# Kernel optimization log

Hardware: AMD Instinct MI355X
Metric: run time of the kernel (lower is better)

Reference implementation:

```python
import jax, jax.numpy as jnp
import numpy as np

DEG = np.float32(np.pi / 180.0)


def _m33(rows):
    # rows: 3 lists of 3 per-batch scalars [B] -> [B,3,3]
    return jnp.stack([jnp.stack(r, axis=-1) for r in rows], axis=-2)


def setup_inputs() -> dict:
    key = jax.random.key(0)
    k1, k2, k3, k4 = jax.random.split(key, 4)
    images = jax.random.uniform(k1, (32, 512, 512, 3), dtype=jnp.float32)
    geom_u = jax.random.uniform(k2, (32, 8), dtype=jnp.float32)
    color_u = jax.random.uniform(k3, (32, 4), dtype=jnp.float32)
    cutout_u = jax.random.uniform(k4, (32, 5), dtype=jnp.float32)
    return {"images": images, "geom_u": geom_u, "color_u": color_u, "cutout_u": cutout_u}


def reference(images, geom_u, color_u, cutout_u):
    B, H, W, C = images.shape
    f32 = jnp.float32

    # --- per-image geometric params (defaults of augment()) ---
    flip = geom_u[:, 0] > 0.5
    tilt = (geom_u[:, 1] * 2 - 1) * (15 * DEG)     # perspective around X
    pan = (geom_u[:, 2] * 2 - 1) * (15 * DEG)      # perspective around Y
    rot = (geom_u[:, 3] * 2 - 1) * (15 * DEG)      # in-plane rotation
    sc = 1.0 + (geom_u[:, 4] * 2 - 1) * 0.1        # isotropic scale
    tx = (geom_u[:, 5] * 2 - 1) * 0.2              # translation (0.1 of image = 0.2 in [-1,1])
    ty = (geom_u[:, 6] * 2 - 1) * 0.2

    z = jnp.zeros_like(rot)
    o = jnp.ones_like(rot)
    fx = jnp.where(flip, f32(-1.0), f32(1.0))
    F = _m33([[fx, z, z], [z, o, z], [z, z, o]])
    ct, st = jnp.cos(tilt), jnp.sin(tilt)
    Rx = _m33([[o, z, z], [z, ct, -st], [z, st, ct]])
    cp, sp = jnp.cos(pan), jnp.sin(pan)
    Ry = _m33([[cp, z, sp], [z, o, z], [-sp, z, cp]])
    cr, sr = jnp.cos(rot), jnp.sin(rot)
    RS = _m33([[sc * cr, -sc * sr, z], [sc * sr, sc * cr, z], [z, z, o]])
    T = _m33([[o, z, tx], [z, o, ty], [z, z, o]])
    # output -> input homography in normalized [-1,1] coords: translation after
    # rotation/scale after perspective after flip (application order of augment())
    M = T @ RS @ Rx @ Ry @ F  # [B,3,3]

    # --- single bilinear resample through the composed homography ---
    ys, xs = jnp.meshgrid(jnp.linspace(-1.0, 1.0, H, dtype=f32),
                          jnp.linspace(-1.0, 1.0, W, dtype=f32), indexing="ij")
    pts = jnp.stack([xs.ravel(), ys.ravel(), jnp.ones(H * W, dtype=f32)], axis=0)  # [3,N]
    src = jnp.einsum("bij,jn->bin", M, pts)  # [B,3,N]
    u = src[:, 0] / src[:, 2]
    v = src[:, 1] / src[:, 2]
    px = (u + 1.0) * 0.5 * (W - 1)
    py = (v + 1.0) * 0.5 * (H - 1)
    valid = (px >= 0) & (px <= W - 1) & (py >= 0) & (py <= H - 1)
    x0 = jnp.clip(jnp.floor(px), 0, W - 1)
    y0 = jnp.clip(jnp.floor(py), 0, H - 1)
    wx = (px - x0)[..., None]
    wy = (py - y0)[..., None]
    x0i = x0.astype(jnp.int32)
    y0i = y0.astype(jnp.int32)
    x1i = jnp.clip(x0i + 1, 0, W - 1)
    y1i = jnp.clip(y0i + 1, 0, H - 1)
    b = jnp.arange(B)[:, None]
    g00 = images[b, y0i, x0i]  # [B,N,3]
    g01 = images[b, y0i, x1i]
    g10 = images[b, y1i, x0i]
    g11 = images[b, y1i, x1i]
    samp = (g00 * (1 - wx) * (1 - wy) + g01 * wx * (1 - wy)
            + g10 * (1 - wx) * wy + g11 * wx * wy)
    samp = samp * valid[..., None].astype(f32)  # zero fill outside
    x = samp.reshape(B, H, W, C)

    # --- color chain: gamma, then fused hue/saturation/brightness matrix ---
    gamma = 1.0 + (color_u[:, 3] * 2 - 1) * 0.2
    x = jnp.power(jnp.clip(x, 0.0, 1.0), gamma[:, None, None, None])

    theta = (color_u[:, 0] * 2 - 1) * (10 * DEG)
    c, s = jnp.cos(theta), jnp.sin(theta)
    a = f32(1.0 / np.sqrt(3.0))
    I3 = jnp.eye(3, dtype=f32)
    K = jnp.array([[0, -a, a], [a, 0, -a], [-a, a, 0]], dtype=f32)  # cross-product w/ gray axis
    A = jnp.full((3, 3), 1.0 / 3.0, dtype=f32)
    Rh = c[:, None, None] * I3 + s[:, None, None] * K + (1 - c)[:, None, None] * A  # hue rotation
    sat = 1.0 + (color_u[:, 1] * 2 - 1) * 0.4
    lum = jnp.array([0.299, 0.587, 0.114], dtype=f32)
    L = jnp.broadcast_to(lum, (3, 3))
    Sm = sat[:, None, None] * I3 + (1 - sat)[:, None, None] * L  # saturation
    bright = 1.0 + (color_u[:, 2] * 2 - 1) * 0.1
    Mc = bright[:, None, None] * (Sm @ Rh)  # [B,3,3]
    x = jnp.clip(jnp.einsum("bhwc,bdc->bhwd", x, Mc), 0.0, 1.0)

    # --- cutout (p=0.5, side in [0.3,0.5] of image) ---
    apply = cutout_u[:, 0] < 0.5
    cx, cy = cutout_u[:, 1], cutout_u[:, 2]
    cw = 0.3 + 0.2 * cutout_u[:, 3]
    ch = 0.3 + 0.2 * cutout_u[:, 4]
    gy, gx = jnp.meshgrid(jnp.linspace(0.0, 1.0, H, dtype=f32),
                          jnp.linspace(0.0, 1.0, W, dtype=f32), indexing="ij")
    mask = (apply[:, None, None]
            & (jnp.abs(gx[None] - cx[:, None, None]) < cw[:, None, None] * 0.5)
            & (jnp.abs(gy[None] - cy[:, None, None]) < ch[:, None, None] * 0.5))
    x = jnp.where(mask[..., None], f32(0.0), x)
    return x
```

## Files before the change

### kernel.cpp

```cpp
#include <hip/hip_runtime.h>
#include <math.h>

#define NB 32
#define HDIM 512
#define WDIM 512
#define HW (HDIM * WDIM)
#define PSTR 32
#define LIN11_OFF 1024
#define LIN01_OFF 1536

struct __attribute__((packed, aligned(4))) F3 { float x, y, z; };

__device__ inline void mm3(float* C, const float* A, const float* B) {
#pragma unroll
  for (int i = 0; i < 3; ++i) {
#pragma unroll
    for (int j = 0; j < 3; ++j) {
      float acc = __fmaf_rn(A[i*3+0], B[0*3+j], 0.0f);
      acc = __fmaf_rn(A[i*3+1], B[1*3+j], acc);
      acc = __fmaf_rn(A[i*3+2], B[2*3+j], acc);
      C[i*3+j] = acc;
    }
  }
}

__global__ void setup_params(const float* __restrict__ geom,
                             const float* __restrict__ color,
                             const float* __restrict__ cut,
                             float* __restrict__ W) {
  const int t = threadIdx.x;
  W[LIN11_OFF + t] = (float)((double)t * (2.0 / 511.0) + (-1.0));
  W[LIN01_OFF + t] = (float)((double)t * (1.0 / 511.0));
  if (t >= NB) return;
  const int b = t;

  const float DEGf = (float)(3.14159265358979323846 / 180.0);
  const float a15  = 15.0f * DEGf;
  const float a10  = 10.0f * DEGf;

  const float* g = geom + b * 8;
  float tilt = __fmul_rn(__fsub_rn(__fmul_rn(g[1], 2.0f), 1.0f), a15);
  float pan  = __fmul_rn(__fsub_rn(__fmul_rn(g[2], 2.0f), 1.0f), a15);
  float rotf = __fmul_rn(__fsub_rn(__fmul_rn(g[3], 2.0f), 1.0f), a15);
  float sc   = __fadd_rn(1.0f,
                 __fmul_rn(__fsub_rn(__fmul_rn(g[4], 2.0f), 1.0f), 0.1f));
  float tx   = __fmul_rn(__fsub_rn(__fmul_rn(g[5], 2.0f), 1.0f), 0.2f);
  float ty   = __fmul_rn(__fsub_rn(__fmul_rn(g[6], 2.0f), 1.0f), 0.2f);
  float fx   = (g[0] > 0.5f) ? -1.0f : 1.0f;

  float ct = (float)cos((double)tilt), st = (float)sin((double)tilt);
  float cp = (float)cos((double)pan),  sp = (float)sin((double)pan);
  float cr = (float)cos((double)rotf), sr = (float)sin((double)rotf);

  float sccr = __fmul_rn(sc, cr);
  float scsr = __fmul_rn(sc, sr);

  float F[9]  = {fx, 0.f, 0.f,  0.f, 1.f, 0.f,  0.f, 0.f, 1.f};
  float Rx[9] = {1.f, 0.f, 0.f,  0.f, ct, -st,  0.f, st, ct};
  float Ry[9] = {cp, 0.f, sp,  0.f, 1.f, 0.f,  -sp, 0.f, cp};
  float RS[9] = {sccr, -scsr, 0.f,  scsr, sccr, 0.f,  0.f, 0.f, 1.f};
  float T[9]  = {1.f, 0.f, tx,  0.f, 1.f, ty,  0.f, 0.f, 1.f};

  float t1[9], t2[9], M[9];
  mm3(t1, T, RS);
  mm3(t2, t1, Rx);
  mm3(t1, t2, Ry);
  mm3(M, t1, F);

  const float* c = color + b * 4;
  float theta  = __fmul_rn(__fsub_rn(__fmul_rn(c[0], 2.0f), 1.0f), a10);
  float sat    = __fadd_rn(1.0f,
                   __fmul_rn(__fsub_rn(__fmul_rn(c[1], 2.0f), 1.0f), 0.4f));
  float bright = __fadd_rn(1.0f,
                   __fmul_rn(__fsub_rn(__fmul_rn(c[2], 2.0f), 1.0f), 0.1f));
  float gammaf = __fadd_rn(1.0f,
                   __fmul_rn(__fsub_rn(__fmul_rn(c[3], 2.0f), 1.0f), 0.2f));

  float cth = (float)cos((double)theta), sth = (float)sin((double)theta);
  float omc = __fsub_rn(1.0f, cth);
  float oms = __fsub_rn(1.0f, sat);
  const float aK = (float)(1.0 / sqrt(3.0));
  const float Af = (float)(1.0 / 3.0);
  const float K[9]   = {0.f, -aK, aK,  aK, 0.f, -aK,  -aK, aK, 0.f};
  const float lum[3] = {(float)0.299, (float)0.587, (float)0.114};

  float Rh[9], Sm[9], SR[9];
#pragma unroll
  for (int i = 0; i < 3; ++i) {
#pragma unroll
    for (int j = 0; j < 3; ++j) {
      float I = (i == j) ? 1.0f : 0.0f;
      Rh[i*3+j] = __fadd_rn(
          __fadd_rn(__fmul_rn(cth, I), __fmul_rn(sth, K[i*3+j])),
          __fmul_rn(omc, Af));
      Sm[i*3+j] = __fadd_rn(__fmul_rn(sat, I), __fmul_rn(oms, lum[j]));
    }
  }
  mm3(SR, Sm, Rh);

  float* pp = W + b * PSTR;
#pragma unroll
  for (int i = 0; i < 9; ++i) pp[i] = M[i];
#pragma unroll
  for (int i = 0; i < 9; ++i) pp[9 + i] = __fmul_rn(bright, SR[i]);
  pp[18] = gammaf;

  const float* cu = cut + b * 5;
  pp[19] = (cu[0] < 0.5f) ? 1.0f : 0.0f;
  pp[20] = cu[1];
  pp[21] = cu[2];
  pp[22] = __fmul_rn(__fadd_rn(0.3f, __fmul_rn(0.2f, cu[3])), 0.5f);
  pp[23] = __fmul_rn(__fadd_rn(0.3f, __fmul_rn(0.2f, cu[4])), 0.5f);
}

__global__ __launch_bounds__(512, 1) void augment_kernel(
    const float* __restrict__ img, const float* __restrict__ W,
    float* __restrict__ out) {
  const int bkid = ((blockIdx.x & 7) << 9) | ((int)blockIdx.x >> 3);
  const int bb = bkid >> 7;
  const int tile = bkid & 127;
  const int t = (int)threadIdx.x;
  const int xx  = ((tile & 15) << 5) | (t & 31);
  const int yy0 = ((tile >> 4) << 6) | ((t >> 5) << 2);

  const float* pp = W + bb * PSTR;
  const float m00 = pp[0], m01 = pp[1], m02 = pp[2];
  const float m10 = pp[3], m11 = pp[4], m12 = pp[5];
  const float m20 = pp[6], m21 = pp[7], m22 = pp[8];

  const float xs = W[LIN11_OFF + xx];
  const float4 ysv = *(const float4*)(W + LIN11_OFF + yy0);
  const float ysa[4] = {ysv.x, ysv.y, ysv.z, ysv.w};

  const float m00xs = __fmul_rn(m00, xs);
  const float m10xs = __fmul_rn(m10, xs);
  const float m20xs = __fmul_rn(m20, xs);

  float wxa[4], wya[4], vma[4];
  int o00[4], o01[4], o10[4], o11[4];
#pragma unroll
  for (int i = 0; i < 4; ++i) {
    const float ys = ysa[i];
    const float s0 = __fadd_rn(
        __fadd_rn(m00xs, __fmul_rn(m01, ys)), m02);
    const float s1 = __fadd_rn(
        __fadd_rn(m10xs, __fmul_rn(m11, ys)), m12);
    const float s2 = __fadd_rn(
        __fadd_rn(m20xs, __fmul_rn(m21, ys)), m22);
    const float u = __fdiv_rn(s0, s2);
    const float v = __fdiv_rn(s1, s2);
    const float px = __fmul_rn(__fmul_rn(__fadd_rn(u, 1.0f), 0.5f), 511.0f);
    const float py = __fmul_rn(__fmul_rn(__fadd_rn(v, 1.0f), 0.5f), 511.0f);

    vma[i] =
        (px >= 0.0f && px <= 511.0f && py >= 0.0f && py <= 511.0f) ? 1.0f
                                                                   : 0.0f;
    const float pxc = __builtin_amdgcn_fmed3f(px, 0.0f, 511.0f);
    const float pyc = __builtin_amdgcn_fmed3f(py, 0.0f, 511.0f);
    const float x0f = floorf(pxc), y0f = floorf(pyc);
    wxa[i] = pxc - x0f;
    wya[i] = pyc - y0f;
    const int x0 = (int)x0f, y0 = (int)y0f;
    const int x1 = min(x0 + 1, WDIM - 1);
    const int y1 = min(y0 + 1, HDIM - 1);
    o00[i] = (y0 * WDIM + x0) * 3;
    o01[i] = (y0 * WDIM + x1) * 3;
    o10[i] = (y1 * WDIM + x0) * 3;
    o11[i] = (y1 * WDIM + x1) * 3;
  }

  const float* base = img + (size_t)bb * (HW * 3);
  F3 g00[4], g01[4], g10[4], g11[4];
#pragma unroll
  for (int i = 0; i < 4; ++i) {
    g00[i] = *(const F3*)(base + o00[i]);
    g01[i] = *(const F3*)(base + o01[i]);
    g10[i] = *(const F3*)(base + o10[i]);
    g11[i] = *(const F3*)(base + o11[i]);
  }
  __builtin_amdgcn_sched_barrier(0);

  const float c00 = pp[9],  c01 = pp[10], c02 = pp[11];
  const float c10 = pp[12], c11 = pp[13], c12 = pp[14];
  const float c20 = pp[15], c21 = pp[16], c22 = pp[17];
  const float gamma = pp[18];
  const float capply = pp[19], ccx = pp[20], ccy = pp[21];
  const float chw = pp[22], chh = pp[23];

  const float gx = W[LIN01_OFF + xx];
  const float4 gyv = *(const float4*)(W + LIN01_OFF + yy0);
  const float gya[4] = {gyv.x, gyv.y, gyv.z, gyv.w};
  const bool cutx = (capply != 0.0f) && (fabsf(__fsub_rn(gx, ccx)) < chw);

  const size_t pix0 = (size_t)bb * HW + (size_t)yy0 * WDIM + xx;
#pragma unroll
  for (int i = 0; i < 4; ++i) {
    const float wx = wxa[i], wy = wya[i], vm = vma[i];
    const float ax = (1.0f - wx) * vm;
    const float bx = wx * vm;
    const float w00 = ax * (1.0f - wy);
    const float w01 = bx * (1.0f - wy);
    const float w10 = ax * wy;
    const float w11 = bx * wy;

    float s, r0, r1, r2;
    s = g00[i].x * w00 + g01[i].x * w01 + g10[i].x * w10 + g11[i].x * w11;
    s = __builtin_amdgcn_fmed3f(s, 0.0f, 1.0f);
    r0 = __builtin_amdgcn_exp2f(gamma * __builtin_amdgcn_logf(s));
    s = g00[i].y * w00 + g01[i].y * w01 + g10[i].y * w10 + g11[i].y * w11;
    s = __builtin_amdgcn_fmed3f(s, 0.0f, 1.0f);
    r1 = __builtin_amdgcn_exp2f(gamma * __builtin_amdgcn_logf(s));
    s = g00[i].z * w00 + g01[i].z * w01 + g10[i].z * w10 + g11[i].z * w11;
    s = __builtin_amdgcn_fmed3f(s, 0.0f, 1.0f);
    r2 = __builtin_amdgcn_exp2f(gamma * __builtin_amdgcn_logf(s));

    float q0 = __builtin_amdgcn_fmed3f(c00 * r0 + c01 * r1 + c02 * r2, 0.0f, 1.0f);
    float q1 = __builtin_amdgcn_fmed3f(c10 * r0 + c11 * r1 + c12 * r2, 0.0f, 1.0f);
    float q2 = __builtin_amdgcn_fmed3f(c20 * r0 + c21 * r1 + c22 * r2, 0.0f, 1.0f);

    const bool cutm = cutx && (fabsf(__fsub_rn(gya[i], ccy)) < chh);
    if (cutm) { q0 = 0.0f; q1 = 0.0f; q2 = 0.0f; }

    F3 o; o.x = q0; o.y = q1; o.z = q2;
    *(F3*)(out + (pix0 + (size_t)i * WDIM) * 3) = o;
  }
}

extern "C" void kernel_launch(void* const* d_in, const int* in_sizes, int n_in,
                              void* d_out, int out_size, void* d_ws, size_t ws_size,
                              hipStream_t stream) {
  const float* images = (const float*)d_in[0];
  const float* geom   = (const float*)d_in[1];
  const float* color  = (const float*)d_in[2];
  const float* cutu   = (const float*)d_in[3];
  float* W = (float*)d_ws;

  setup_params<<<1, 512, 0, stream>>>(geom, color, cutu, W);

  const int npix = NB * HW;
  augment_kernel<<<npix / 2048, 512, 0, stream>>>(images, W, (float*)d_out);
}
```

Baseline: 41.04 us.

## Vectorize homography and blend math with packed f32x2, use fast reciprocal division

Replaces the two IEEE-correct divisions per pixel with one fast reciprocal plus a Newton refinement, computed on packed float2 vectors so the compiler can emit packed FP32 instructions. When a sample lands within a quarter pixel of the image border it falls back to exact division, to keep the validity mask and clamping identical. Bilinear blending and the colour-matrix multiply are also partly packed, and the neighbour offsets are built from one base plus conditional deltas. The fast-path coordinates can differ by an ulp from the exact ones away from the border, and the border branch adds divergence.

Result: slower. 44.24 us (+7.8%).

```diff
diff --git a/kernel.cpp b/kernel.cpp
--- a/kernel.cpp
+++ b/kernel.cpp
@@ -8,8 +8,12 @@
 #define PSTR 32
 #define LIN11_OFF 1024
 #define LIN01_OFF 1536
+#define NEARD 0.25f
 
 struct __attribute__((packed, aligned(4))) F3 { float x, y, z; };
+typedef float f32x2 __attribute__((ext_vector_type(2)));
+
+static __device__ __forceinline__ f32x2 sp(float v) { return (f32x2){v, v}; }
 
 __device__ inline void mm3(float* C, const float* A, const float* B) {
 #pragma unroll
@@ -49,7 +53,7 @@
   float fx   = (g[0] > 0.5f) ? -1.0f : 1.0f;
 
   float ct = (float)cos((double)tilt), st = (float)sin((double)tilt);
-  float cp = (float)cos((double)pan),  sp = (float)sin((double)pan);
+  float cp = (float)cos((double)pan),  sp_ = (float)sin((double)pan);
   float cr = (float)cos((double)rotf), sr = (float)sin((double)rotf);
 
   float sccr = __fmul_rn(sc, cr);
@@ -57,7 +61,7 @@
 
   float F[9]  = {fx, 0.f, 0.f,  0.f, 1.f, 0.f,  0.f, 0.f, 1.f};
   float Rx[9] = {1.f, 0.f, 0.f,  0.f, ct, -st,  0.f, st, ct};
-  float Ry[9] = {cp, 0.f, sp,  0.f, 1.f, 0.f,  -sp, 0.f, cp};
+  float Ry[9] = {cp, 0.f, sp_,  0.f, 1.f, 0.f,  -sp_, 0.f, cp};
   float RS[9] = {sccr, -scsr, 0.f,  scsr, sccr, 0.f,  0.f, 0.f, 1.f};
   float T[9]  = {1.f, 0.f, tx,  0.f, 1.f, ty,  0.f, 0.f, 1.f};
 
@@ -130,28 +134,65 @@
 
   const float xs = W[LIN11_OFF + xx];
   const float4 ysv = *(const float4*)(W + LIN11_OFF + yy0);
-  const float ysa[4] = {ysv.x, ysv.y, ysv.z, ysv.w};
 
   const float m00xs = __fmul_rn(m00, xs);
   const float m10xs = __fmul_rn(m10, xs);
   const float m20xs = __fmul_rn(m20, xs);
 
+  float pxa[4], pya[4];
+  {
+    const f32x2 vm01 = sp(m01), vm11 = sp(m11), vm21 = sp(m21);
+    const f32x2 vm02 = sp(m02), vm12 = sp(m12), vm22 = sp(m22);
+    const f32x2 vm00xs = sp(m00xs), vm10xs = sp(m10xs), vm20xs = sp(m20xs);
+#pragma unroll
+    for (int p = 0; p < 2; ++p) {
+      const f32x2 ys = p ? (f32x2){ysv.z, ysv.w} : (f32x2){ysv.x, ysv.y};
+      f32x2 s0, s1, s2;
+      {
+#pragma clang fp contract(off)
+        s0 = (vm00xs + vm01 * ys) + vm02;
+        s1 = (vm10xs + vm11 * ys) + vm12;
+        s2 = (vm20xs + vm21 * ys) + vm22;
+      }
+      f32x2 r = {__builtin_amdgcn_rcpf(s2.x), __builtin_amdgcn_rcpf(s2.y)};
+      const f32x2 e = __builtin_elementwise_fma(-s2, r, sp(1.0f));
+      r = __builtin_elementwise_fma(e, r, r);
+      f32x2 px2, py2;
+      {
+#pragma clang fp contract(off)
+        const f32x2 u = s0 * r;
+        const f32x2 v = s1 * r;
+        px2 = ((u + sp(1.0f)) * sp(0.5f)) * sp(511.0f);
+        py2 = ((v + sp(1.0f)) * sp(0.5f)) * sp(511.0f);
+      }
+#pragma unroll
+      for (int h = 0; h < 2; ++h) {
+        const int i = p * 2 + h;
+        float px = h ? px2.y : px2.x;
+        float py = h ? py2.y : py2.x;
+        const bool nearb =
+            (fabsf(px) < NEARD) || (fabsf(px - 511.0f) < NEARD) ||
+            (fabsf(py) < NEARD) || (fabsf(py - 511.0f) < NEARD);
+        if (nearb) {
+          const float S0 = h ? s0.y : s0.x;
+          const float S1 = h ? s1.y : s1.x;
+          const float S2 = h ? s2.y : s2.x;
+          const float ue = __fdiv_rn(S0, S2);
+          const float ve = __fdiv_rn(S1, S2);
+          px = __fmul_rn(__fmul_rn(__fadd_rn(ue, 1.0f), 0.5f), 511.0f);
+          py = __fmul_rn(__fmul_rn(__fadd_rn(ve, 1.0f), 0.5f), 511.0f);
+        }
+        pxa[i] = px;
+        pya[i] = py;
+      }
+    }
+  }
+
   float wxa[4], wya[4], vma[4];
   int o00[4], o01[4], o10[4], o11[4];
 #pragma unroll
   for (int i = 0; i < 4; ++i) {
-    const float ys = ysa[i];
-    const float s0 = __fadd_rn(
-        __fadd_rn(m00xs, __fmul_rn(m01, ys)), m02);
-    const float s1 = __fadd_rn(
-        __fadd_rn(m10xs, __fmul_rn(m11, ys)), m12);
-    const float s2 = __fadd_rn(
-        __fadd_rn(m20xs, __fmul_rn(m21, ys)), m22);
-    const float u = __fdiv_rn(s0, s2);
-    const float v = __fdiv_rn(s1, s2);
-    const float px = __fmul_rn(__fmul_rn(__fadd_rn(u, 1.0f), 0.5f), 511.0f);
-    const float py = __fmul_rn(__fmul_rn(__fadd_rn(v, 1.0f), 0.5f), 511.0f);
-
+    const float px = pxa[i], py = pya[i];
     vma[i] =
         (px >= 0.0f && px <= 511.0f && py >= 0.0f && py <= 511.0f) ? 1.0f
                                                                    : 0.0f;
@@ -161,12 +202,13 @@
     wxa[i] = pxc - x0f;
     wya[i] = pyc - y0f;
     const int x0 = (int)x0f, y0 = (int)y0f;
-    const int x1 = min(x0 + 1, WDIM - 1);
-    const int y1 = min(y0 + 1, HDIM - 1);
-    o00[i] = (y0 * WDIM + x0) * 3;
-    o01[i] = (y0 * WDIM + x1) * 3;
-    o10[i] = (y1 * WDIM + x0) * 3;
-    o11[i] = (y1 * WDIM + x1) * 3;
+    const int o = (y0 * WDIM + x0) * 3;
+    const int dx = (x0 < WDIM - 1) ? 3 : 0;
+    const int dy = (y0 < HDIM - 1) ? WDIM * 3 : 0;
+    o00[i] = o;
+    o01[i] = o + dx;
+    o10[i] = o + dy;
+    o11[i] = o + dy + dx;
   }
 
   const float* base = img + (size_t)bb * (HW * 3);
@@ -180,8 +222,9 @@
   }
   __builtin_amdgcn_sched_barrier(0);
 
-  const float c00 = pp[9],  c01 = pp[10], c02 = pp[11];
-  const float c10 = pp[12], c11 = pp[13], c12 = pp[14];
+  const f32x2 cA = {pp[9], pp[12]};
+  const f32x2 cB = {pp[10], pp[13]};
+  const f32x2 cC = {pp[11], pp[14]};
   const float c20 = pp[15], c21 = pp[16], c22 = pp[17];
   const float gamma = pp[18];
   const float capply = pp[19], ccx = pp[20], ccy = pp[21];
@@ -198,25 +241,30 @@
     const float wx = wxa[i], wy = wya[i], vm = vma[i];
     const float ax = (1.0f - wx) * vm;
     const float bx = wx * vm;
-    const float w00 = ax * (1.0f - wy);
-    const float w01 = bx * (1.0f - wy);
-    const float w10 = ax * wy;
-    const float w11 = bx * wy;
-
-    float s, r0, r1, r2;
-    s = g00[i].x * w00 + g01[i].x * w01 + g10[i].x * w10 + g11[i].x * w11;
-    s = __builtin_amdgcn_fmed3f(s, 0.0f, 1.0f);
-    r0 = __builtin_amdgcn_exp2f(gamma * __builtin_amdgcn_logf(s));
-    s = g00[i].y * w00 + g01[i].y * w01 + g10[i].y * w10 + g11[i].y * w11;
-    s = __builtin_amdgcn_fmed3f(s, 0.0f, 1.0f);
-    r1 = __builtin_amdgcn_exp2f(gamma * __builtin_amdgcn_logf(s));
-    s = g00[i].z * w00 + g01[i].z * w01 + g10[i].z * w10 + g11[i].z * w11;
-    s = __builtin_amdgcn_fmed3f(s, 0.0f, 1.0f);
-    r2 = __builtin_amdgcn_exp2f(gamma * __builtin_amdgcn_logf(s));
-
-    float q0 = __builtin_amdgcn_fmed3f(c00 * r0 + c01 * r1 + c02 * r2, 0.0f, 1.0f);
-    float q1 = __builtin_amdgcn_fmed3f(c10 * r0 + c11 * r1 + c12 * r2, 0.0f, 1.0f);
-    float q2 = __builtin_amdgcn_fmed3f(c20 * r0 + c21 * r1 + c22 * r2, 0.0f, 1.0f);
+    const float omwy = 1.0f - wy;
+    const float w00 = ax * omwy, w01 = bx * omwy;
+    const float w10 = ax * wy,   w11 = bx * wy;
+
+    const f32x2 gxy00 = {g00[i].x, g00[i].y};
+    const f32x2 gxy01 = {g01[i].x, g01[i].y};
+    const f32x2 gxy10 = {g10[i].x, g10[i].y};
+    const f32x2 gxy11 = {g11[i].x, g11[i].y};
+    f32x2 sxy =
+        gxy00 * sp(w00) + gxy01 * sp(w01) + gxy10 * sp(w10) + gxy11 * sp(w11);
+    float sz = g00[i].z * w00 + g01[i].z * w01 + g10[i].z * w10 + g11[i].z * w11;
+
+    const float sx = __builtin_amdgcn_fmed3f(sxy.x, 0.0f, 1.0f);
+    const float sy = __builtin_amdgcn_fmed3f(sxy.y, 0.0f, 1.0f);
+    sz = __builtin_amdgcn_fmed3f(sz, 0.0f, 1.0f);
+    const float r0 = __builtin_amdgcn_exp2f(gamma * __builtin_amdgcn_logf(sx));
+    const float r1 = __builtin_amdgcn_exp2f(gamma * __builtin_amdgcn_logf(sy));
+    const float r2 = __builtin_amdgcn_exp2f(gamma * __builtin_amdgcn_logf(sz));
+
+    f32x2 q01 = cA * sp(r0) + cB * sp(r1) + cC * sp(r2);
+    float q2v = c20 * r0 + c21 * r1 + c22 * r2;
+    float q0 = __builtin_amdgcn_fmed3f(q01.x, 0.0f, 1.0f);
+    float q1 = __builtin_amdgcn_fmed3f(q01.y, 0.0f, 1.0f);
+    float q2 = __builtin_amdgcn_fmed3f(q2v, 0.0f, 1.0f);
 
     const bool cutm = cutx && (fabsf(__fsub_rn(gya[i], ccy)) < chh);
     if (cutm) { q0 = 0.0f; q1 = 0.0f; q2 = 0.0f; }
```
